# Performance work log

Measured on AMD Instinct MI355X. Metric: run time of the kernel, lower is better.

## Reference

```python
import jax, jax.numpy as jnp
import numpy as np

OUTDIM = 10
STRIDES = (2, 2, 1)
PADS = (2, 2, 1)  # int((k-1)/2) for k=5,5,3
LEAK = 0.2


def _conv(x, w, b, s, p):
    y = jax.lax.conv_general_dilated(x, w, (s, s), [(p, p), (p, p)],
                                     dimension_numbers=('NCHW', 'OIHW', 'NCHW'))
    return y + b[None, :, None, None]


def _grid(outdim):
    off = (jnp.arange(outdim, dtype=jnp.float32) - (outdim - 1) / 2.0) / outdim
    gx = jnp.broadcast_to(off[None, :], (outdim, outdim))  # varies along j (x)
    gy = jnp.broadcast_to(off[:, None], (outdim, outdim))  # varies along i (y)
    return jnp.stack([gx, gy], axis=-1)  # [od, od, 2]


def _bilinear(img, x, y):
    # img: [C,H,W]; x,y: [N] float. Faithful to original (x clamped by H, y by W).
    H, W = img.shape[-2], img.shape[-1]
    x0 = jnp.floor(x).astype(jnp.int32); x1 = x0 + 1
    y0 = jnp.floor(y).astype(jnp.int32); y1 = y0 + 1
    x0 = jnp.clip(x0, 0, H - 1); x1 = jnp.clip(x1, 0, H - 1)
    y0 = jnp.clip(y0, 0, W - 1); y1 = jnp.clip(y1, 0, W - 1)
    Ia = img[:, y0, x0]; Ib = img[:, y1, x0]; Ic = img[:, y0, x1]; Id = img[:, y1, x1]
    x0f = x0.astype(x.dtype); x1f = x1.astype(x.dtype)
    y0f = y0.astype(y.dtype); y1f = y1.astype(y.dtype)
    step = jnp.clip((x1f - x0f) * (y1f - y0f), 0.001, 2.0)
    inv = 1.0 / step
    wa = (x1f - x) * (y1f - y) * inv
    wb = (x1f - x) * (y - y0f) * inv
    wc = (x - x0f) * (y1f - y) * inv
    wd = (x - x0f) * (y - y0f) * inv
    return Ia * wa + Ib * wb + Ic * wc + Id * wd  # [C, N]


def _roi_one(feat, roi, gg):
    # feat: [C,H,W]; roi: [R,7]
    W1, W2 = roi[:, 2:3], roi[:, 3:4]
    H1, H2 = roi[:, 4:5], roi[:, 5:6]
    psi = roi[:, 6:7]
    WH = jnp.concatenate([W1 + W2, H1 + H2], axis=-1)          # [R,2]
    offset = jnp.concatenate([(W1 - W2) / 2, (H1 - H2) / 2], axis=-1)
    s, c = jnp.sin(psi), jnp.cos(psi)                          # [R,1]
    rotM = jnp.stack([jnp.concatenate([c, -s], -1),
                      jnp.concatenate([s, c], -1)], axis=-2)   # [R,2,2]
    ggi = gg[None] * WH[:, None, None, :] - offset[:, None, None, :]  # [R,od,od,2]
    ggi = jnp.einsum('rijk,rkl->rijl', ggi, rotM) + roi[:, None, None, 0:2]
    xs = ggi[..., 0].reshape(-1)
    ys = ggi[..., 1].reshape(-1)
    samp = _bilinear(feat, xs, ys)                             # [C, R*od*od]
    R, C = roi.shape[0], feat.shape[0]
    # faithful to original .view(R, C, od, od) applied to the [C, N] buffer
    return samp.reshape(R, C, OUTDIM, OUTDIM)


def setup_inputs() -> dict:
    key = jax.random.key(0)
    ks = jax.random.split(key, 12)
    B, R = 32, 32
    x = jax.random.normal(ks[0], (B, 3, 224, 224), dtype=jnp.float32)
    u = jax.random.uniform(ks[1], (B, R, 7), dtype=jnp.float32)
    lo = jnp.array([5., 5., 1., 1., 1., 1., -np.pi], dtype=jnp.float32)
    hi = jnp.array([51., 51., 8., 8., 8., 8., np.pi], dtype=jnp.float32)
    ROI = lo + u * (hi - lo)  # coords in 56x56 feature-map frame
    w1 = jax.random.normal(ks[2], (32, 3, 5, 5), dtype=jnp.float32) * 0.05
    b1 = jnp.zeros((32,), dtype=jnp.float32)
    w2 = jax.random.normal(ks[3], (64, 32, 5, 5), dtype=jnp.float32) * 0.05
    b2 = jnp.zeros((64,), dtype=jnp.float32)
    w3 = jax.random.normal(ks[4], (128, 64, 3, 3), dtype=jnp.float32) * 0.05
    b3 = jnp.zeros((128,), dtype=jnp.float32)
    fc_w = jax.random.normal(ks[5], (256, OUTDIM * OUTDIM * 128), dtype=jnp.float32) * 0.01
    fc_b = jnp.zeros((256,), dtype=jnp.float32)
    return {'x': x, 'ROI': ROI, 'w1': w1, 'b1': b1, 'w2': w2, 'b2': b2,
            'w3': w3, 'b3': b3, 'fc_w': fc_w, 'fc_b': fc_b}


def reference(x, ROI, w1, b1, w2, b2, w3, b3, fc_w, fc_b):
    for (w, b, s, p) in ((w1, b1, STRIDES[0], PADS[0]),
                         (w2, b2, STRIDES[1], PADS[1]),
                         (w3, b3, STRIDES[2], PADS[2])):
        x = jax.nn.leaky_relu(_conv(x, w, b, s, p), LEAK)
    gg = _grid(OUTDIM)
    roi_feat = jax.vmap(lambda f, r: _roi_one(f, r, gg))(x, ROI)  # [B,R,C,od,od]
    B, R = roi_feat.shape[0], roi_feat.shape[1]
    flat = roi_feat.reshape(B, R, -1)
    return flat @ fc_w.T + fc_b  # [B, R, 256]
```

## Files before the change

kernel.cpp:

```cpp
#include <hip/hip_runtime.h>
#include <hip/hip_bf16.h>

#define LEAK 0.2f

__device__ __forceinline__ float lrelu(float a) { return a > 0.0f ? a : LEAK * a; }

typedef __attribute__((ext_vector_type(8))) short short8;
typedef __attribute__((ext_vector_type(4))) float f32x4;

__device__ __forceinline__ unsigned short bf16_hi_bits(float x) {
    unsigned u = __builtin_bit_cast(unsigned, x);
    unsigned r = u + 0x7fffu + ((u >> 16) & 1u);
    return (unsigned short)(r >> 16);
}
__device__ __forceinline__ float bf16_to_f32(unsigned short h) {
    unsigned u = ((unsigned)h) << 16;
    return __builtin_bit_cast(float, u);
}
__device__ __forceinline__ unsigned pack_bf16pair(float x) {
    unsigned short h = bf16_hi_bits(x);
    float lo = x - bf16_to_f32(h);
    return (unsigned)h | ((unsigned)bf16_hi_bits(lo) << 16);
}

__device__ __forceinline__ unsigned pack_lo16(unsigned o, unsigned e) {
    return __builtin_amdgcn_perm(o, e, 0x05040100u);
}
__device__ __forceinline__ unsigned pack_hi16(unsigned o, unsigned e) {
    return __builtin_amdgcn_perm(o, e, 0x07060302u);
}

template<int CO, int KIN, int KP>
__global__ __launch_bounds__(256) void wtr_pack_k(const float* __restrict__ w,
                                                  unsigned* __restrict__ wTp) {
    int i = blockIdx.x * 256 + threadIdx.x;
    if (i >= KP * CO) return;
    int k = i / CO, co = i % CO;
    float x = (k < KIN) ? w[(size_t)co * KIN + k] : 0.0f;
    wTp[i] = pack_bf16pair(x);
}

__global__ __launch_bounds__(256) void split_pack_k(const float* __restrict__ src,
                                                    unsigned* __restrict__ dst, int n) {
    for (int i = blockIdx.x * 256 + threadIdx.x; i < n; i += gridDim.x * 256) {
        dst[i] = pack_bf16pair(src[i]);
    }
}

__global__ __launch_bounds__(256, 4) void conv1_mfma_k(
    const unsigned* __restrict__ src,
    const unsigned* __restrict__ wp,
    const float* __restrict__ bias,
    unsigned* __restrict__ outp)
{
    __shared__ unsigned ldsu[6400];
    __shared__ int offtab[96];
    short* const lds = (short*)ldsu;

    const int tid  = threadIdx.x;
    const int lane = tid & 63;
    const int wv   = tid >> 6;
    const int bx   = blockIdx.x;
    const int bz   = blockIdx.y;

    if (tid < 96) {
        int k = min(tid, 74);
        int ci = k / 25, r = k - ci * 25;
        int kh = r / 5, kw = r - kh * 5;
        offtab[tid] = (ci * 228 + kh) * 228 + kw;
    }
    __syncthreads();

    const int brow = tid & 127, half = tid >> 7;
    const int bn   = bx * 128 + brow;
    const int boh  = bn / 112, bow = bn % 112;
    const unsigned* __restrict__ bsrc =
        src + ((size_t)(bz * 3) * 228 + boh * 2) * 228 + bow * 2;
    const int arow = tid & 31, ks = (tid >> 5) & 3;

    unsigned Bu[16], Au[8];
    auto gather = [&](int it) {
        const int k0 = it * 32;
#pragma unroll
        for (int c = 0; c < 2; ++c) {
            int kb = k0 + (half * 2 + c) * 8;
            int4 o0 = *(const int4*)&offtab[kb];
            int4 o1 = *(const int4*)&offtab[kb + 4];
            Bu[c * 8 + 0] = bsrc[o0.x]; Bu[c * 8 + 1] = bsrc[o0.y];
            Bu[c * 8 + 2] = bsrc[o0.z]; Bu[c * 8 + 3] = bsrc[o0.w];
            Bu[c * 8 + 4] = bsrc[o1.x]; Bu[c * 8 + 5] = bsrc[o1.y];
            Bu[c * 8 + 6] = bsrc[o1.z]; Bu[c * 8 + 7] = bsrc[o1.w];
        }
        if (tid < 128) {
            const unsigned* __restrict__ wk = wp + (size_t)(k0 + ks * 8) * 32 + arow;
#pragma unroll
            for (int j = 0; j < 8; ++j) Au[j] = wk[j * 32];
        }
    };

    f32x4 acc[2][2] = {};
    const int r15 = lane & 15, kg = lane >> 4;

    gather(0);
    for (int it = 0; it < 3; ++it) {
        {
            uint4 vh, vl;
#pragma unroll
            for (int c = 0; c < 2; ++c) {
                vh.x = pack_lo16(Bu[c*8+1], Bu[c*8+0]); vl.x = pack_hi16(Bu[c*8+1], Bu[c*8+0]);
                vh.y = pack_lo16(Bu[c*8+3], Bu[c*8+2]); vl.y = pack_hi16(Bu[c*8+3], Bu[c*8+2]);
                vh.z = pack_lo16(Bu[c*8+5], Bu[c*8+4]); vl.z = pack_hi16(Bu[c*8+5], Bu[c*8+4]);
                vh.w = pack_lo16(Bu[c*8+7], Bu[c*8+6]); vl.w = pack_hi16(Bu[c*8+7], Bu[c*8+6]);
                *(uint4*)&ldsu[1280 + brow * 20 + (half * 2 + c) * 4] = vh;
                *(uint4*)&ldsu[3840 + brow * 20 + (half * 2 + c) * 4] = vl;
            }
            if (tid < 128) {
                vh.x = pack_lo16(Au[1], Au[0]); vl.x = pack_hi16(Au[1], Au[0]);
                vh.y = pack_lo16(Au[3], Au[2]); vl.y = pack_hi16(Au[3], Au[2]);
                vh.z = pack_lo16(Au[5], Au[4]); vl.z = pack_hi16(Au[5], Au[4]);
                vh.w = pack_lo16(Au[7], Au[6]); vl.w = pack_hi16(Au[7], Au[6]);
                *(uint4*)&ldsu[arow * 20 + ks * 4]       = vh;
                *(uint4*)&ldsu[640 + arow * 20 + ks * 4] = vl;
            }
        }
        __syncthreads();
        if (it + 1 < 3) gather(it + 1);

        const short* AsH = lds;
        const short* AsL = lds + 1280;
        const short* BsH = lds + 2560;
        const short* BsL = lds + 7680;
        short8 aH[2], aL[2], bH[2], bL[2];
#pragma unroll
        for (int tq = 0; tq < 2; ++tq) {
            const int ra = (tq * 16 + r15) * 40 + kg * 8;
            aH[tq] = *(const short8*)&AsH[ra];
            aL[tq] = *(const short8*)&AsL[ra];
            const int rb = (wv * 32 + tq * 16 + r15) * 40 + kg * 8;
            bH[tq] = *(const short8*)&BsH[rb];
            bL[tq] = *(const short8*)&BsL[rb];
        }
#pragma unroll
        for (int ct = 0; ct < 2; ++ct)
#pragma unroll
            for (int pt = 0; pt < 2; ++pt) {
                acc[ct][pt] = __builtin_amdgcn_mfma_f32_16x16x32_bf16(aH[ct], bH[pt], acc[ct][pt], 0, 0, 0);
                acc[ct][pt] = __builtin_amdgcn_mfma_f32_16x16x32_bf16(aH[ct], bL[pt], acc[ct][pt], 0, 0, 0);
                acc[ct][pt] = __builtin_amdgcn_mfma_f32_16x16x32_bf16(aL[ct], bH[pt], acc[ct][pt], 0, 0, 0);
            }
        __syncthreads();
    }

#pragma unroll
    for (int ct = 0; ct < 2; ++ct)
#pragma unroll
        for (int pt = 0; pt < 2; ++pt)
#pragma unroll
            for (int rg = 0; rg < 4; ++rg) {
                int co = ct * 16 + kg * 4 + rg;
                int px = bx * 128 + wv * 32 + pt * 16 + r15;
                int poh = px / 112, pw_ = px % 112;
                float v = acc[ct][pt][rg] + bias[co];
                outp[((size_t)(bz * 32 + co) * 116 + poh + 2) * 120 + pw_ + 4] =
                    pack_bf16pair(lrelu(v));
            }
}

template<int CI, int ST, int KH, int KW, int KP,
         int PIH, int PIW, int LP,
         int CO, int OW, int OSH, int OSW, int OR0, int OC0, bool POUT>
__global__ __launch_bounds__(256, 4) void conv_mfma_k(
    const unsigned* __restrict__ src,
    const unsigned* __restrict__ wp,
    const float* __restrict__ bias,
    void* __restrict__ outv)
{
    constexpr int KT = KP / 32;
    __shared__ unsigned ldsu[5120];
    __shared__ int offtab[KP];
    short* const lds = (short*)ldsu;

    const int tid  = threadIdx.x;
    const int lane = tid & 63;
    const int wv   = tid >> 6;
    const int bx   = blockIdx.x;
    const int by   = blockIdx.y;
    const int bz   = blockIdx.z;

    for (int k = tid; k < KP; k += 256) {
        int ci = k / (KH * KW), r = k - ci * (KH * KW);
        int kh = r / KW, kw = r - kh * KW;
        offtab[k] = (ci * PIH + kh) * PIW + kw;
    }
    __syncthreads();

    const int row = lane;
    const int n   = bx * 64 + row;
    const int oh  = n / OW, ow = n % OW;
    const unsigned* __restrict__ bsrc =
        src + ((size_t)(bz * CI) * PIH + oh * ST) * PIW + ow * ST + LP;
    const unsigned* __restrict__ wsrc = wp + (size_t)(wv * 8) * CO + by * 64 + row;

    unsigned Au[8], Bu[8];
    auto gatherA = [&](int it) {
        const unsigned* __restrict__ wk = wsrc + (size_t)it * 32 * CO;
#pragma unroll
        for (int j = 0; j < 8; ++j) Au[j] = wk[j * CO];
    };
    auto gatherB = [&](int4 o0, int4 o1) {
        Bu[0] = bsrc[o0.x]; Bu[1] = bsrc[o0.y]; Bu[2] = bsrc[o0.z]; Bu[3] = bsrc[o0.w];
        Bu[4] = bsrc[o1.x]; Bu[5] = bsrc[o1.y]; Bu[6] = bsrc[o1.z]; Bu[7] = bsrc[o1.w];
    };

    f32x4 acc[2][2] = {};

    const int cw = wv & 1, pw = wv >> 1;
    const int r15 = lane & 15, kg = lane >> 4;

    int4 o0 = *(const int4*)&offtab[wv * 8];
    int4 o1 = *(const int4*)&offtab[wv * 8 + 4];
    gatherA(0); gatherB(o0, o1);
    for (int it = 0; it < KT; ++it) {
        int4 n0, n1;
        if (it + 1 < KT) {
            const int nk = (it + 1) * 32 + wv * 8;
            n0 = *(const int4*)&offtab[nk];
            n1 = *(const int4*)&offtab[nk + 4];
        }
        {
            const int widx = row * 20 + wv * 4;
            uint4 vh, vl;
            vh.x = pack_lo16(Au[1], Au[0]); vl.x = pack_hi16(Au[1], Au[0]);
            vh.y = pack_lo16(Au[3], Au[2]); vl.y = pack_hi16(Au[3], Au[2]);
            vh.z = pack_lo16(Au[5], Au[4]); vl.z = pack_hi16(Au[5], Au[4]);
            vh.w = pack_lo16(Au[7], Au[6]); vl.w = pack_hi16(Au[7], Au[6]);
            *(uint4*)&ldsu[0 * 1280 + widx] = vh;
            *(uint4*)&ldsu[1 * 1280 + widx] = vl;
            vh.x = pack_lo16(Bu[1], Bu[0]); vl.x = pack_hi16(Bu[1], Bu[0]);
            vh.y = pack_lo16(Bu[3], Bu[2]); vl.y = pack_hi16(Bu[3], Bu[2]);
            vh.z = pack_lo16(Bu[5], Bu[4]); vl.z = pack_hi16(Bu[5], Bu[4]);
            vh.w = pack_lo16(Bu[7], Bu[6]); vl.w = pack_hi16(Bu[7], Bu[6]);
            *(uint4*)&ldsu[2 * 1280 + widx] = vh;
            *(uint4*)&ldsu[3 * 1280 + widx] = vl;
        }
        __syncthreads();
        if (it + 1 < KT) { gatherA(it + 1); gatherB(n0, n1); }

        const short* AsH = lds + 0 * 2560;
        const short* AsL = lds + 1 * 2560;
        const short* BsH = lds + 2 * 2560;
        const short* BsL = lds + 3 * 2560;
        short8 aH[2], aL[2], bH[2], bL[2];
#pragma unroll
        for (int tq = 0; tq < 2; ++tq) {
            const int ra = (cw * 32 + tq * 16 + r15) * 40 + kg * 8;
            aH[tq] = *(const short8*)&AsH[ra];
            aL[tq] = *(const short8*)&AsL[ra];
            const int rb = (pw * 32 + tq * 16 + r15) * 40 + kg * 8;
            bH[tq] = *(const short8*)&BsH[rb];
            bL[tq] = *(const short8*)&BsL[rb];
        }
#pragma unroll
        for (int ct = 0; ct < 2; ++ct)
#pragma unroll
            for (int pt = 0; pt < 2; ++pt) {
                acc[ct][pt] = __builtin_amdgcn_mfma_f32_16x16x32_bf16(aH[ct], bH[pt], acc[ct][pt], 0, 0, 0);
                acc[ct][pt] = __builtin_amdgcn_mfma_f32_16x16x32_bf16(aH[ct], bL[pt], acc[ct][pt], 0, 0, 0);
                acc[ct][pt] = __builtin_amdgcn_mfma_f32_16x16x32_bf16(aL[ct], bH[pt], acc[ct][pt], 0, 0, 0);
            }
        __syncthreads();
    }

#pragma unroll
    for (int ct = 0; ct < 2; ++ct)
#pragma unroll
        for (int pt = 0; pt < 2; ++pt)
#pragma unroll
            for (int rg = 0; rg < 4; ++rg) {
                int co = by * 64 + cw * 32 + ct * 16 + kg * 4 + rg;
                int px = bx * 64 + pw * 32 + pt * 16 + r15;
                int poh = px / OW, pow_ = px % OW;
                float v = lrelu(acc[ct][pt][rg] + bias[co]);
                size_t off = ((size_t)(bz * CO + co) * OSH + (poh + OR0)) * OSW + (pow_ + OC0);
                if (POUT) ((unsigned*)outv)[off] = pack_bf16pair(v);
                else      ((float*)outv)[off]    = v;
            }
}

__global__ __launch_bounds__(256, 4) void fc_mfma_k(
    const unsigned* __restrict__ Sp,
    const unsigned* __restrict__ Wp,
    float* __restrict__ part)
{
    __shared__ unsigned ldsu[7680];
    short* const lds = (short*)ldsu;

    const int tid  = threadIdx.x;
    const int lane = tid & 63;
    const int wv   = tid >> 6;
    const int bn = blockIdx.x, bm = blockIdx.y, ks = blockIdx.z;

    const int ra = tid & 127, ca = tid >> 7;
    const int rb = tid & 63,  cb = tid >> 6;
    const unsigned* __restrict__ aptr = Sp + (size_t)(bm * 128 + ra) * 12800 + ks * 800;
    const unsigned* __restrict__ bptr = Wp + (size_t)(bn * 64 + rb) * 12800 + ks * 800;

    unsigned Au[16], Bu[8];
    auto gather = [&](int it) {
        const int k0 = it * 32;
#pragma unroll
        for (int j = 0; j < 8; ++j) {
            Au[j]     = aptr[k0 + ca * 8 + j];
            Au[8 + j] = aptr[k0 + (ca + 2) * 8 + j];
            Bu[j]     = bptr[k0 + cb * 8 + j];
        }
    };

    f32x4 acc[2][4] = {};
    const int r15 = lane & 15, kg = lane >> 4;

    gather(0);
    for (int it = 0; it < 25; ++it) {
        {
            uint4 vh, vl;
            vh.x = pack_lo16(Au[1], Au[0]); vl.x = pack_hi16(Au[1], Au[0]);
            vh.y = pack_lo16(Au[3], Au[2]); vl.y = pack_hi16(Au[3], Au[2]);
            vh.z = pack_lo16(Au[5], Au[4]); vl.z = pack_hi16(Au[5], Au[4]);
            vh.w = pack_lo16(Au[7], Au[6]); vl.w = pack_hi16(Au[7], Au[6]);
            *(uint4*)&ldsu[ra * 20 + ca * 4]        = vh;
            *(uint4*)&ldsu[2560 + ra * 20 + ca * 4] = vl;
            vh.x = pack_lo16(Au[9],  Au[8]);  vl.x = pack_hi16(Au[9],  Au[8]);
            vh.y = pack_lo16(Au[11], Au[10]); vl.y = pack_hi16(Au[11], Au[10]);
            vh.z = pack_lo16(Au[13], Au[12]); vl.z = pack_hi16(Au[13], Au[12]);
            vh.w = pack_lo16(Au[15], Au[14]); vl.w = pack_hi16(Au[15], Au[14]);
            *(uint4*)&ldsu[ra * 20 + (ca + 2) * 4]        = vh;
            *(uint4*)&ldsu[2560 + ra * 20 + (ca + 2) * 4] = vl;
            vh.x = pack_lo16(Bu[1], Bu[0]); vl.x = pack_hi16(Bu[1], Bu[0]);
            vh.y = pack_lo16(Bu[3], Bu[2]); vl.y = pack_hi16(Bu[3], Bu[2]);
            vh.z = pack_lo16(Bu[5], Bu[4]); vl.z = pack_hi16(Bu[5], Bu[4]);
            vh.w = pack_lo16(Bu[7], Bu[6]); vl.w = pack_hi16(Bu[7], Bu[6]);
            *(uint4*)&ldsu[5120 + rb * 20 + cb * 4] = vh;
            *(uint4*)&ldsu[6400 + rb * 20 + cb * 4] = vl;
        }
        __syncthreads();
        if (it + 1 < 25) gather(it + 1);

        const short* AsH = lds;
        const short* AsL = AsH + 5120;
        const short* BsH = AsH + 10240;
        const short* BsL = AsH + 12800;
        short8 aH[2], aL[2], bH[4], bL[4];
#pragma unroll
        for (int mq = 0; mq < 2; ++mq) {
            const int rr = (wv * 32 + mq * 16 + r15) * 40 + kg * 8;
            aH[mq] = *(const short8*)&AsH[rr];
            aL[mq] = *(const short8*)&AsL[rr];
        }
#pragma unroll
        for (int nq = 0; nq < 4; ++nq) {
            const int rr = (nq * 16 + r15) * 40 + kg * 8;
            bH[nq] = *(const short8*)&BsH[rr];
            bL[nq] = *(const short8*)&BsL[rr];
        }
#pragma unroll
        for (int mq = 0; mq < 2; ++mq)
#pragma unroll
            for (int nq = 0; nq < 4; ++nq) {
                acc[mq][nq] = __builtin_amdgcn_mfma_f32_16x16x32_bf16(aH[mq], bH[nq], acc[mq][nq], 0, 0, 0);
                acc[mq][nq] = __builtin_amdgcn_mfma_f32_16x16x32_bf16(aH[mq], bL[nq], acc[mq][nq], 0, 0, 0);
                acc[mq][nq] = __builtin_amdgcn_mfma_f32_16x16x32_bf16(aL[mq], bH[nq], acc[mq][nq], 0, 0, 0);
            }
        __syncthreads();
    }

    float* __restrict__ po = part + (size_t)ks * 262144;
#pragma unroll
    for (int mq = 0; mq < 2; ++mq)
#pragma unroll
        for (int nq = 0; nq < 4; ++nq)
#pragma unroll
            for (int rg = 0; rg < 4; ++rg) {
                int m = bm * 128 + wv * 32 + mq * 16 + kg * 4 + rg;
                int ncol = bn * 64 + nq * 16 + r15;
                po[(size_t)m * 256 + ncol] = acc[mq][nq][rg];
            }
}

__global__ __launch_bounds__(256) void pad_x_k(const float* __restrict__ x,
                                               unsigned* __restrict__ xp) {
    int blk = blockIdx.x;
    int r4 = blk % 57, ic = blk / 57;
    int wid = threadIdx.x >> 6, lane = threadIdx.x & 63;
    int row = r4 * 4 + wid;
    const float* __restrict__ src = x + (size_t)ic * 224 * 224 + (size_t)(row - 2) * 224;
    unsigned* __restrict__ dst = xp + (size_t)ic * 228 * 228 + (size_t)row * 228;
    bool rok = (row >= 2) && (row < 226);
    for (int c = lane; c < 228; c += 64) {
        float v = 0.0f;
        if (rok && c >= 2 && c < 226) v = src[c - 2];
        dst[c] = pack_bf16pair(v);
    }
}

__global__ __launch_bounds__(256) void zb_c1p_k(float* __restrict__ p) {
    float* base = p + (size_t)blockIdx.x * (116 * 120);
    for (int t = threadIdx.x; t < 928; t += 256) {
        int idx;
        if (t < 480) {
            int r = t / 120, c = t - r * 120;
            int row = (r < 2) ? r : r + 112;
            idx = row * 120 + c;
        } else {
            int s = t - 480;
            int r = s >> 2, c = s & 3;
            int col = (c < 2) ? (c + 2) : (c + 114);
            idx = (r + 2) * 120 + col;
        }
        base[idx] = 0.0f;
    }
}

__global__ __launch_bounds__(64) void zb_c2p_k(float* __restrict__ p) {
    float* base = p + (size_t)blockIdx.x * (58 * 64);
    for (int t = threadIdx.x; t < 240; t += 64) {
        int idx;
        if (t < 128) {
            int r = t >> 6, c = t & 63;
            idx = (r ? 57 : 0) * 64 + c;
        } else {
            int s = t - 128;
            int r = (s >> 1) + 1;
            idx = r * 64 + ((s & 1) ? 60 : 3);
        }
        base[idx] = 0.0f;
    }
}

__global__ __launch_bounds__(256) void roi_k(const float* __restrict__ feat,
                                             const float* __restrict__ roi,
                                             unsigned* __restrict__ S) {
    int b = blockIdx.x >> 5;
    int r = blockIdx.x & 31;
    const float* rr = roi + (size_t)(b * 32 + r) * 7;

    __shared__ int   offA[100], offB[100], offC[100], offD[100];
    __shared__ float wA[100], wB[100], wC[100], wD[100];

    int tid = threadIdx.x;
    if (tid < 100) {
        int i = tid / 10, j = tid % 10;
        float cx = rr[0], cy = rr[1];
        float W1 = rr[2], W2 = rr[3], H1 = rr[4], H2 = rr[5], psi = rr[6];
        float offx = ((float)j - 4.5f) / 10.0f;
        float offy = ((float)i - 4.5f) / 10.0f;
        float gx = offx * (W1 + W2) - (W1 - W2) * 0.5f;
        float gy = offy * (H1 + H2) - (H1 - H2) * 0.5f;
        float sn = sinf(psi), cs = cosf(psi);
        float xs = gx * cs + gy * sn + cx;
        float ys = -gx * sn + gy * cs + cy;

        float x0f = floorf(xs), y0f = floorf(ys);
        int x0 = (int)x0f, x1 = x0 + 1;
        int y0 = (int)y0f, y1 = y0 + 1;
        x0 = min(max(x0, 0), 55); x1 = min(max(x1, 0), 55);
        y0 = min(max(y0, 0), 55); y1 = min(max(y1, 0), 55);
        float fx0 = (float)x0, fx1 = (float)x1;
        float fy0 = (float)y0, fy1 = (float)y1;
        float step = (fx1 - fx0) * (fy1 - fy0);
        step = fminf(fmaxf(step, 0.001f), 2.0f);
        float inv = 1.0f / step;
        wA[tid] = (fx1 - xs) * (fy1 - ys) * inv;
        wB[tid] = (fx1 - xs) * (ys - fy0) * inv;
        wC[tid] = (xs - fx0) * (fy1 - ys) * inv;
        wD[tid] = (xs - fx0) * (ys - fy0) * inv;
        offA[tid] = y0 * 56 + x0;
        offB[tid] = y1 * 56 + x0;
        offC[tid] = y0 * 56 + x1;
        offD[tid] = y1 * 56 + x1;
    }
    __syncthreads();

    const float* __restrict__ fb = feat + (size_t)b * 128 * 3136;
    unsigned* __restrict__ outb = S + ((size_t)b * 128 * 32 + r) * 100;
    int c = tid / 100;
    int p = tid - c * 100;
    for (int t = tid; t < 12800; t += 256) {
        const float* f = fb + c * 3136;
        float v = wA[p] * f[offA[p]] + wB[p] * f[offB[p]] +
                  wC[p] * f[offC[p]] + wD[p] * f[offD[p]];
        outb[(size_t)c * 3200 + p] = pack_bf16pair(v);
        p += 56; c += 2;
        if (p >= 100) { p -= 100; ++c; }
    }
}

__global__ __launch_bounds__(256) void fc2_reduce_k(const float* __restrict__ part,
                                                    const float* __restrict__ bias,
                                                    float* __restrict__ out) {
    int i = blockIdx.x * 256 + threadIdx.x;
    float s = bias[i & 255];
    for (int ks = 0; ks < 16; ++ks) s += part[(size_t)ks * 262144 + i];
    out[i] = s;
}

extern "C" void kernel_launch(void* const* d_in, const int* in_sizes, int n_in,
                              void* d_out, int out_size, void* d_ws, size_t ws_size,
                              hipStream_t stream) {
    const float* x   = (const float*)d_in[0];
    const float* ROI = (const float*)d_in[1];
    const float* w1  = (const float*)d_in[2];
    const float* b1  = (const float*)d_in[3];
    const float* w2  = (const float*)d_in[4];
    const float* b2  = (const float*)d_in[5];
    const float* w3  = (const float*)d_in[6];
    const float* b3  = (const float*)d_in[7];
    const float* fcw = (const float*)d_in[8];
    const float* fcb = (const float*)d_in[9];
    float* out = (float*)d_out;

    char* ws = (char*)d_ws;
    unsigned* c1p  = (unsigned*)(ws);
    unsigned* c2p  = (unsigned*)(ws + 57016320);
    unsigned* xpad = (unsigned*)(ws + 87425024);
    unsigned* wT1p = (unsigned*)(ws + 107386880);
    unsigned* wT2p = (unsigned*)(ws + 107399168);
    unsigned* wT3p = (unsigned*)(ws + 107603968);
    float* c3   = (float*)(ws);
    unsigned* S = (unsigned*)(ws + 57016320);
    unsigned* wfcp = (unsigned*)(ws);
    float* part = (float*)(ws + 16777216);

    wtr_pack_k<32, 75, 96><<<12, 256, 0, stream>>>(w1, wT1p);
    wtr_pack_k<64, 800, 800><<<200, 256, 0, stream>>>(w2, wT2p);
    wtr_pack_k<128, 576, 576><<<288, 256, 0, stream>>>(w3, wT3p);
    pad_x_k<<<32 * 3 * 57, 256, 0, stream>>>(x, xpad);
    zb_c1p_k<<<1024, 256, 0, stream>>>((float*)c1p);
    zb_c2p_k<<<2048, 64, 0, stream>>>((float*)c2p);

    conv1_mfma_k<<<dim3(98, 32), 256, 0, stream>>>(xpad, wT1p, b1, c1p);

    conv_mfma_k<32, 2, 5, 5, 800, 116, 120, 2, 64, 56, 58, 64, 1, 4, true>
        <<<dim3(49, 1, 32), 256, 0, stream>>>(c1p, wT2p, b2, c2p);

    conv_mfma_k<64, 1, 3, 3, 576, 58, 64, 3, 128, 56, 56, 56, 0, 0, false>
        <<<dim3(49, 2, 32), 256, 0, stream>>>(c2p, wT3p, b3, c3);

    roi_k<<<1024, 256, 0, stream>>>(c3, ROI, S);
    split_pack_k<<<4096, 256, 0, stream>>>(fcw, wfcp, 3276800);
    fc_mfma_k<<<dim3(4, 8, 16), 256, 0, stream>>>(S, wfcp, part);
    fc2_reduce_k<<<1024, 256, 0, stream>>>(part, fcb, out);
}
```

Before: 370.7 us.

## Widen conv3 output-channel tile to reuse im2col gather; split roi_k channels

```diff
diff --git a/kernel.cpp b/kernel.cpp
--- a/kernel.cpp
+++ b/kernel.cpp
@@ -168,15 +168,16 @@
 
 template<int CI, int ST, int KH, int KW, int KP,
          int PIH, int PIW, int LP,
-         int CO, int OW, int OSH, int OSW, int OR0, int OC0, bool POUT>
+         int CO, int OW, int OSH, int OSW, int OR0, int OC0, bool POUT, int CT>
 __global__ __launch_bounds__(256, 4) void conv_mfma_k(
     const unsigned* __restrict__ src,
     const unsigned* __restrict__ wp,
     const float* __restrict__ bias,
     void* __restrict__ outv)
 {
-    constexpr int KT = KP / 32;
-    __shared__ unsigned ldsu[5120];
+    constexpr int KT  = KP / 32;
+    constexpr int COB = CT * 64;
+    __shared__ unsigned ldsu[CT * 2560 + 2560];
     __shared__ int offtab[KP];
     short* const lds = (short*)ldsu;
 
@@ -199,20 +200,22 @@
     const int oh  = n / OW, ow = n % OW;
     const unsigned* __restrict__ bsrc =
         src + ((size_t)(bz * CI) * PIH + oh * ST) * PIW + ow * ST + LP;
-    const unsigned* __restrict__ wsrc = wp + (size_t)(wv * 8) * CO + by * 64 + row;
-
-    unsigned Au[8], Bu[8];
+    const unsigned* __restrict__ wsrc = wp + (size_t)(wv * 8) * CO + by * COB + row;
+
+    unsigned Au[CT][8], Bu[8];
     auto gatherA = [&](int it) {
         const unsigned* __restrict__ wk = wsrc + (size_t)it * 32 * CO;
 #pragma unroll
-        for (int j = 0; j < 8; ++j) Au[j] = wk[j * CO];
+        for (int c2 = 0; c2 < CT; ++c2)
+#pragma unroll
+            for (int j = 0; j < 8; ++j) Au[c2][j] = wk[j * CO + c2 * 64];
     };
     auto gatherB = [&](int4 o0, int4 o1) {
         Bu[0] = bsrc[o0.x]; Bu[1] = bsrc[o0.y]; Bu[2] = bsrc[o0.z]; Bu[3] = bsrc[o0.w];
         Bu[4] = bsrc[o1.x]; Bu[5] = bsrc[o1.y]; Bu[6] = bsrc[o1.z]; Bu[7] = bsrc[o1.w];
     };
 
-    f32x4 acc[2][2] = {};
+    f32x4 acc[CT][2][2] = {};
 
     const int cw = wv & 1, pw = wv >> 1;
     const int r15 = lane & 15, kg = lane >> 4;
@@ -228,63 +231,76 @@
             n1 = *(const int4*)&offtab[nk + 4];
         }
         {
-            const int widx = row * 20 + wv * 4;
             uint4 vh, vl;
-            vh.x = pack_lo16(Au[1], Au[0]); vl.x = pack_hi16(Au[1], Au[0]);
-            vh.y = pack_lo16(Au[3], Au[2]); vl.y = pack_hi16(Au[3], Au[2]);
-            vh.z = pack_lo16(Au[5], Au[4]); vl.z = pack_hi16(Au[5], Au[4]);
-            vh.w = pack_lo16(Au[7], Au[6]); vl.w = pack_hi16(Au[7], Au[6]);
-            *(uint4*)&ldsu[0 * 1280 + widx] = vh;
-            *(uint4*)&ldsu[1 * 1280 + widx] = vl;
+#pragma unroll
+            for (int c2 = 0; c2 < CT; ++c2) {
+                const int aidx = (c2 * 64 + row) * 20 + wv * 4;
+                vh.x = pack_lo16(Au[c2][1], Au[c2][0]); vl.x = pack_hi16(Au[c2][1], Au[c2][0]);
+                vh.y = pack_lo16(Au[c2][3], Au[c2][2]); vl.y = pack_hi16(Au[c2][3], Au[c2][2]);
+                vh.z = pack_lo16(Au[c2][5], Au[c2][4]); vl.z = pack_hi16(Au[c2][5], Au[c2][4]);
+                vh.w = pack_lo16(Au[c2][7], Au[c2][6]); vl.w = pack_hi16(Au[c2][7], Au[c2][6]);
+                *(uint4*)&ldsu[aidx]             = vh;
+                *(uint4*)&ldsu[CT * 1280 + aidx] = vl;
+            }
+            const int bidx = 2 * CT * 1280 + row * 20 + wv * 4;
             vh.x = pack_lo16(Bu[1], Bu[0]); vl.x = pack_hi16(Bu[1], Bu[0]);
             vh.y = pack_lo16(Bu[3], Bu[2]); vl.y = pack_hi16(Bu[3], Bu[2]);
             vh.z = pack_lo16(Bu[5], Bu[4]); vl.z = pack_hi16(Bu[5], Bu[4]);
             vh.w = pack_lo16(Bu[7], Bu[6]); vl.w = pack_hi16(Bu[7], Bu[6]);
-            *(uint4*)&ldsu[2 * 1280 + widx] = vh;
-            *(uint4*)&ldsu[3 * 1280 + widx] = vl;
+            *(uint4*)&ldsu[bidx]        = vh;
+            *(uint4*)&ldsu[bidx + 1280] = vl;
         }
         __syncthreads();
         if (it + 1 < KT) { gatherA(it + 1); gatherB(n0, n1); }
 
-        const short* AsH = lds + 0 * 2560;
-        const short* AsL = lds + 1 * 2560;
-        const short* BsH = lds + 2 * 2560;
-        const short* BsL = lds + 3 * 2560;
-        short8 aH[2], aL[2], bH[2], bL[2];
+        const short* AsH = lds;
+        const short* AsL = lds + CT * 2560;
+        const short* BsH = lds + 2 * CT * 2560;
+        const short* BsL = BsH + 2560;
+        short8 bH[2], bL[2];
 #pragma unroll
         for (int tq = 0; tq < 2; ++tq) {
-            const int ra = (cw * 32 + tq * 16 + r15) * 40 + kg * 8;
-            aH[tq] = *(const short8*)&AsH[ra];
-            aL[tq] = *(const short8*)&AsL[ra];
             const int rb = (pw * 32 + tq * 16 + r15) * 40 + kg * 8;
             bH[tq] = *(const short8*)&BsH[rb];
             bL[tq] = *(const short8*)&BsL[rb];
         }
 #pragma unroll
+        for (int c2 = 0; c2 < CT; ++c2) {
+            short8 aH[2], aL[2];
+#pragma unroll
+            for (int tq = 0; tq < 2; ++tq) {
+                const int ra = (c2 * 64 + cw * 32 + tq * 16 + r15) * 40 + kg * 8;
+                aH[tq] = *(const short8*)&AsH[ra];
+                aL[tq] = *(const short8*)&AsL[ra];
+            }
+#pragma unroll
+            for (int ct = 0; ct < 2; ++ct)
+#pragma unroll
+                for (int pt = 0; pt < 2; ++pt) {
+                    acc[c2][ct][pt] = __builtin_amdgcn_mfma_f32_16x16x32_bf16(aH[ct], bH[pt], acc[c2][ct][pt], 0, 0, 0);
+                    acc[c2][ct][pt] = __builtin_amdgcn_mfma_f32_16x16x32_bf16(aH[ct], bL[pt], acc[c2][ct][pt], 0, 0, 0);
+                    acc[c2][ct][pt] = __builtin_amdgcn_mfma_f32_16x16x32_bf16(aL[ct], bH[pt], acc[c2][ct][pt], 0, 0, 0);
+                }
+        }
+        __syncthreads();
+    }
+
+#pragma unroll
+    for (int c2 = 0; c2 < CT; ++c2)
+#pragma unroll
         for (int ct = 0; ct < 2; ++ct)
 #pragma unroll
-            for (int pt = 0; pt < 2; ++pt) {
-                acc[ct][pt] = __builtin_amdgcn_mfma_f32_16x16x32_bf16(aH[ct], bH[pt], acc[ct][pt], 0, 0, 0);
-                acc[ct][pt] = __builtin_amdgcn_mfma_f32_16x16x32_bf16(aH[ct], bL[pt], acc[ct][pt], 0, 0, 0);
-                acc[ct][pt] = __builtin_amdgcn_mfma_f32_16x16x32_bf16(aL[ct], bH[pt], acc[ct][pt], 0, 0, 0);
-            }
-        __syncthreads();
-    }
-
-#pragma unroll
-    for (int ct = 0; ct < 2; ++ct)
-#pragma unroll
-        for (int pt = 0; pt < 2; ++pt)
-#pragma unroll
-            for (int rg = 0; rg < 4; ++rg) {
-                int co = by * 64 + cw * 32 + ct * 16 + kg * 4 + rg;
-                int px = bx * 64 + pw * 32 + pt * 16 + r15;
-                int poh = px / OW, pow_ = px % OW;
-                float v = lrelu(acc[ct][pt][rg] + bias[co]);
-                size_t off = ((size_t)(bz * CO + co) * OSH + (poh + OR0)) * OSW + (pow_ + OC0);
-                if (POUT) ((unsigned*)outv)[off] = pack_bf16pair(v);
-                else      ((float*)outv)[off]    = v;
-            }
+            for (int pt = 0; pt < 2; ++pt)
+#pragma unroll
+                for (int rg = 0; rg < 4; ++rg) {
+                    int co = by * COB + c2 * 64 + cw * 32 + ct * 16 + kg * 4 + rg;
+                    int px = bx * 64 + pw * 32 + pt * 16 + r15;
+                    int poh = px / OW, pow_ = px % OW;
+                    float v = lrelu(acc[c2][ct][pt][rg] + bias[co]);
+                    size_t off = ((size_t)(bz * CO + co) * OSH + (poh + OR0)) * OSW + (pow_ + OC0);
+                    if (POUT) ((unsigned*)outv)[off] = pack_bf16pair(v);
+                    else      ((float*)outv)[off]    = v;
+                }
 }
 
 __global__ __launch_bounds__(256, 4) void fc_mfma_k(
@@ -441,6 +457,7 @@
                                              unsigned* __restrict__ S) {
     int b = blockIdx.x >> 5;
     int r = blockIdx.x & 31;
+    int z = blockIdx.y;
     const float* rr = roi + (size_t)(b * 32 + r) * 7;
 
     __shared__ int   offA[100], offB[100], offC[100], offD[100];
@@ -482,15 +499,13 @@
 
     const float* __restrict__ fb = feat + (size_t)b * 128 * 3136;
     unsigned* __restrict__ outb = S + ((size_t)b * 128 * 32 + r) * 100;
-    int c = tid / 100;
-    int p = tid - c * 100;
-    for (int t = tid; t < 12800; t += 256) {
+    for (int t = tid; t < 6400; t += 256) {
+        int c = z * 64 + t / 100;
+        int p = t % 100;
         const float* f = fb + c * 3136;
         float v = wA[p] * f[offA[p]] + wB[p] * f[offB[p]] +
                   wC[p] * f[offC[p]] + wD[p] * f[offD[p]];
         outb[(size_t)c * 3200 + p] = pack_bf16pair(v);
-        p += 56; c += 2;
-        if (p >= 100) { p -= 100; ++c; }
     }
 }
 
@@ -539,13 +554,13 @@
 
     conv1_mfma_k<<<dim3(98, 32), 256, 0, stream>>>(xpad, wT1p, b1, c1p);
 
-    conv_mfma_k<32, 2, 5, 5, 800, 116, 120, 2, 64, 56, 58, 64, 1, 4, true>
+    conv_mfma_k<32, 2, 5, 5, 800, 116, 120, 2, 64, 56, 58, 64, 1, 4, true, 1>
         <<<dim3(49, 1, 32), 256, 0, stream>>>(c1p, wT2p, b2, c2p);
 
-    conv_mfma_k<64, 1, 3, 3, 576, 58, 64, 3, 128, 56, 56, 56, 0, 0, false>
-        <<<dim3(49, 2, 32), 256, 0, stream>>>(c2p, wT3p, b3, c3);
-
-    roi_k<<<1024, 256, 0, stream>>>(c3, ROI, S);
+    conv_mfma_k<64, 1, 3, 3, 576, 58, 64, 3, 128, 56, 56, 56, 0, 0, false, 2>
+        <<<dim3(49, 1, 32), 256, 0, stream>>>(c2p, wT3p, b3, c3);
+
+    roi_k<<<dim3(1024, 2), 256, 0, stream>>>(c3, ROI, S);
     split_pack_k<<<4096, 256, 0, stream>>>(fcw, wfcp, 3276800);
     fc_mfma_k<<<dim3(4, 8, 16), 256, 0, stream>>>(S, wfcp, part);
     fc2_reduce_k<<<1024, 256, 0, stream>>>(part, fcb, out);
```

Result: no change. 366.3 us (-1.2%).
